# Performance work log

Measured on AMD Instinct MI355X. Metric: run time of the kernel, lower is better.

Reference implementation:

```python
import jax, jax.numpy as jnp
import numpy as np

N, IN_CH, OUT_CH = 8192, 128, 64

def setup_inputs() -> dict:
    key = jax.random.key(0)
    k1, k2, k3, k4, k5 = jax.random.split(key, 5)
    features = jax.random.normal(k1, (N, IN_CH), dtype=jnp.float32)
    weight_matrix = jax.random.normal(k2, (IN_CH, OUT_CH), dtype=jnp.float32) * (1.0 / np.sqrt(IN_CH))
    filt = jax.random.uniform(k3, (N,), dtype=jnp.float32, minval=0.9, maxval=1.1)
    wavelets = jax.random.normal(k4, (N, N), dtype=jnp.float32) * (1.0 / np.sqrt(N))
    wavelets_inv = jax.random.normal(k5, (N, N), dtype=jnp.float32) * (1.0 / np.sqrt(N))
    return {"features": features, "weight_matrix": weight_matrix, "filt": filt,
            "wavelets": wavelets, "wavelets_inv": wavelets_inv}

def reference(features, weight_matrix, filt, wavelets, wavelets_inv):
    # transformed = features @ W                      [N, out_ch]
    transformed = features @ weight_matrix
    # spectral = wavelets_inv @ transformed           [N, out_ch]
    spectral = wavelets_inv @ transformed
    # wavelets @ diag(filt) == wavelets * filt[None, :] (fused broadcast,
    # mathematically identical to the original dense-diag GEMM)
    out = (wavelets * filt[None, :]) @ spectral
    return out
```

## Files before the change

### kernel.cpp

```cpp
#include <hip/hip_runtime.h>
#include <hip/hip_bf16.h>


typedef unsigned short u16;
typedef short s16x8 __attribute__((ext_vector_type(8)));
typedef float f32x4 __attribute__((ext_vector_type(4)));

__device__ __forceinline__ u16 f2bf(float f) {
    unsigned u;
    __builtin_memcpy(&u, &f, 4);
    unsigned r = (u + 0x7fffu + ((u >> 16) & 1u)) >> 16;
    return (u16)r;
}
__device__ __forceinline__ unsigned pk2(float a, float b) {
    __hip_bfloat162 h = __float22bfloat162_rn(float2{a, b});
    unsigned u;
    __builtin_memcpy(&u, &h, 4);
    return u;
}

#define GAS(p) ((const __attribute__((address_space(1))) void*)(p))
#define LAS(p) ((__attribute__((address_space(3))) void*)(p))

#define NN 8192
#define MT 64
#define BK 64

__global__ __launch_bounds__(256) void k1_feat(const float* __restrict__ F,
                                               const float* __restrict__ W,
                                               float* __restrict__ Tmp) {
    const int tid = threadIdx.x;
    const int col = tid & 63;
    const int rq = tid >> 6;
    const int row0 = blockIdx.x * 16 + rq * 4;
    float a0 = 0.f, a1 = 0.f, a2 = 0.f, a3 = 0.f;
    const float* f0 = F + (size_t)row0 * 128;
    for (int k = 0; k < 128; ++k) {
        float wv = W[k * 64 + col];
        a0 += f0[k] * wv;
        a1 += f0[128 + k] * wv;
        a2 += f0[256 + k] * wv;
        a3 += f0[384 + k] * wv;
    }
    Tmp[(size_t)(row0 + 0) * 64 + col] = a0;
    Tmp[(size_t)(row0 + 1) * 64 + col] = a1;
    Tmp[(size_t)(row0 + 2) * 64 + col] = a2;
    Tmp[(size_t)(row0 + 3) * 64 + col] = a3;
}

__global__ __launch_bounds__(256) void k2_transpose(const float* __restrict__ Tmp,
                                                    u16* __restrict__ Tt) {
    __shared__ u16 s[64][65];
    const int tid = threadIdx.x;
    const int r0 = blockIdx.x * 64;
    const int c = tid & 63, r = tid >> 6;
#pragma unroll
    for (int p = 0; p < 16; ++p)
        s[r + p * 4][c] = f2bf(Tmp[(size_t)(r0 + r + p * 4) * 64 + c]);
    __syncthreads();
    const int j = tid & 63, nq = tid >> 6;
#pragma unroll
    for (int p = 0; p < 16; ++p) {
        int n = nq + p * 4;
        Tt[(size_t)n * NN + r0 + j] = s[j][n];
    }
}

__global__ __launch_bounds__(256) void gemm_af32_bt(const float* __restrict__ A,
                                                    const u16* __restrict__ Bt,
                                                    float* __restrict__ P,
                                                    int kslice) {
    __shared__ __align__(16) u16 As[MT * BK];
    __shared__ __align__(16) u16 Bs[MT * BK];
    const int tid = threadIdx.x;
    const int w = tid >> 6;
    const int l = tid & 63;
    const int m0 = blockIdx.x * MT;
    const int s = blockIdx.y;
    const int k0 = s * kslice;

    f32x4 acc[4] = {f32x4{0,0,0,0}, f32x4{0,0,0,0}, f32x4{0,0,0,0}, f32x4{0,0,0,0}};

    const int ar = tid >> 2;
    const int ac = tid & 3;
    const float* Ap = A + (size_t)(m0 + ar) * NN + (size_t)k0 + ac * 16;
    u16* Arow = As + ar * 64;
    const int g0 = (2 * ac) ^ (ar & 7);
    const int g1 = (2 * ac + 1) ^ (ar & 7);

    const int lr = l >> 3;
    const int lc = (l & 7) ^ lr;
    const u16* Bb = Bt + (size_t)(w * 16 + lr) * NN + lc * 8 + k0;
    char* BsB = (char*)Bs + (w * 16) * 128;

    const int fm = w * 16 + (l & 15);
    const int q = l >> 4;

    for (int kt = 0; kt < kslice; kt += BK) {
        __builtin_amdgcn_global_load_lds(GAS(Bb + kt), LAS(BsB), 16, 0, 0);
        __builtin_amdgcn_global_load_lds(GAS(Bb + kt + 8 * NN), LAS(BsB + 1024), 16, 0, 0);
        f32x4 f0 = *(const f32x4*)(Ap + kt);
        f32x4 f1 = *(const f32x4*)(Ap + kt + 4);
        f32x4 f2 = *(const f32x4*)(Ap + kt + 8);
        f32x4 f3 = *(const f32x4*)(Ap + kt + 12);
        uint4 p0{pk2(f0.x, f0.y), pk2(f0.z, f0.w), pk2(f1.x, f1.y), pk2(f1.z, f1.w)};
        uint4 p1{pk2(f2.x, f2.y), pk2(f2.z, f2.w), pk2(f3.x, f3.y), pk2(f3.z, f3.w)};
        *(uint4*)(Arow + g0 * 8) = p0;
        *(uint4*)(Arow + g1 * 8) = p1;
        __syncthreads();
#pragma unroll
        for (int kk = 0; kk < 2; ++kk) {
            const int acg = (kk * 4 + q) ^ (fm & 7);
            s16x8 af = *(const s16x8*)&As[fm * 64 + acg * 8];
#pragma unroll
            for (int ng = 0; ng < 4; ++ng) {
                const int bn = ng * 16 + (l & 15);
                const int bc = (kk * 4 + q) ^ (bn & 7);
                s16x8 bf = *(const s16x8*)&Bs[bn * 64 + bc * 8];
                acc[ng] = __builtin_amdgcn_mfma_f32_16x16x32_bf16(af, bf, acc[ng], 0, 0, 0);
            }
        }
        __syncthreads();
    }

    float* Pp = P + (size_t)s * NN * 64;
    const int row = m0 + w * 16 + (l >> 4) * 4;
    const int col = l & 15;
#pragma unroll
    for (int ng = 0; ng < 4; ++ng)
#pragma unroll
        for (int r = 0; r < 4; ++r)
            Pp[(size_t)(row + r) * 64 + ng * 16 + col] = acc[ng][r];
}

__global__ __launch_bounds__(256) void k4_reduce_scale_t(const float* __restrict__ P,
                                                         const float* __restrict__ filt,
                                                         u16* __restrict__ St,
                                                         int split) {
    __shared__ u16 s[64][65];
    const int tid = threadIdx.x;
    const int j0 = blockIdx.x * 64;
    const int n = tid & 63, jq = tid >> 6;
#pragma unroll 4
    for (int p = 0; p < 16; ++p) {
        int j = jq + p * 4;
        float acc = 0.f;
        for (int t = 0; t < split; ++t)
            acc += P[((size_t)t * NN + j0 + j) * 64 + n];
        acc *= filt[j0 + j];
        s[j][n] = f2bf(acc);
    }
    __syncthreads();
    const int jj = tid & 63, nq = tid >> 6;
#pragma unroll
    for (int p = 0; p < 16; ++p) {
        int nn = nq + p * 4;
        St[(size_t)nn * NN + j0 + jj] = s[jj][nn];
    }
}

__global__ __launch_bounds__(256) void k6_reduce_out(const float* __restrict__ P,
                                                     float* __restrict__ out,
                                                     int split) {
    const int idx = blockIdx.x * 256 + threadIdx.x;
    float acc = 0.f;
    for (int t = 0; t < split; ++t)
        acc += P[(size_t)t * NN * 64 + idx];
    out[idx] = acc;
}

extern "C" void kernel_launch(void* const* d_in, const int* in_sizes, int n_in,
                              void* d_out, int out_size, void* d_ws, size_t ws_size,
                              hipStream_t stream) {
    const float* F    = (const float*)d_in[0];
    const float* W    = (const float*)d_in[1];
    const float* filt = (const float*)d_in[2];
    const float* Wav  = (const float*)d_in[3];
    const float* Winv = (const float*)d_in[4];
    float* out = (float*)d_out;

    char* ws = (char*)d_ws;
    u16* Tt = (u16*)ws;
    u16* St = (u16*)(ws + (1u << 20));
    float* Tmp = (float*)(ws + (2u << 20));
    float* P   = (float*)(ws + (2u << 20));

    size_t per = (size_t)NN * 64 * 4;
    size_t avail = (ws_size > (2u << 20)) ? ws_size - (2u << 20) : per;
    int maxs = (int)(avail / per);
    if (maxs < 1) maxs = 1;
    int split = 1;
    while (split * 2 <= maxs && split < 8) split *= 2;
    int kslice = NN / split;

    k1_feat<<<512, 256, 0, stream>>>(F, W, Tmp);
    k2_transpose<<<128, 256, 0, stream>>>(Tmp, Tt);
    gemm_af32_bt<<<dim3(128, split), 256, 0, stream>>>(Winv, Tt, P, kslice);
    k4_reduce_scale_t<<<128, 256, 0, stream>>>(P, filt, St, split);
    gemm_af32_bt<<<dim3(128, split), 256, 0, stream>>>(Wav, St, P, kslice);
    k6_reduce_out<<<2048, 256, 0, stream>>>(P, out, split);
}
```

Measured before the change: 653.5 us.

## Double-buffer LDS tiles in split-K GEMM and vectorize feature loads

The GEMM main loop now uses two LDS buffers per operand. The next tile's global loads (direct-to-LDS for B, register loads for A) are issued before computing MFMAs on the current tile, so memory latency overlaps compute and one barrier per iteration is removed. The small features@W kernel also reads feature rows with 16-byte vector loads instead of scalar ones. This doubles LDS usage (32KB per block), which may lower occupancy, and keeps A-tile values live in registers across the MFMA section.

```diff
diff --git a/kernel.cpp b/kernel.cpp
--- a/kernel.cpp
+++ b/kernel.cpp
@@ -35,12 +35,19 @@
     const int row0 = blockIdx.x * 16 + rq * 4;
     float a0 = 0.f, a1 = 0.f, a2 = 0.f, a3 = 0.f;
     const float* f0 = F + (size_t)row0 * 128;
-    for (int k = 0; k < 128; ++k) {
-        float wv = W[k * 64 + col];
-        a0 += f0[k] * wv;
-        a1 += f0[128 + k] * wv;
-        a2 += f0[256 + k] * wv;
-        a3 += f0[384 + k] * wv;
+    for (int k = 0; k < 128; k += 4) {
+        f32x4 v0 = *(const f32x4*)(f0 + k);
+        f32x4 v1 = *(const f32x4*)(f0 + 128 + k);
+        f32x4 v2 = *(const f32x4*)(f0 + 256 + k);
+        f32x4 v3 = *(const f32x4*)(f0 + 384 + k);
+#pragma unroll
+        for (int kk = 0; kk < 4; ++kk) {
+            float wv = W[(k + kk) * 64 + col];
+            a0 += v0[kk] * wv;
+            a1 += v1[kk] * wv;
+            a2 += v2[kk] * wv;
+            a3 += v3[kk] * wv;
+        }
     }
     Tmp[(size_t)(row0 + 0) * 64 + col] = a0;
     Tmp[(size_t)(row0 + 1) * 64 + col] = a1;
@@ -70,8 +77,8 @@
                                                     const u16* __restrict__ Bt,
                                                     float* __restrict__ P,
                                                     int kslice) {
-    __shared__ __align__(16) u16 As[MT * BK];
-    __shared__ __align__(16) u16 Bs[MT * BK];
+    __shared__ __align__(16) u16 As[2][MT * BK];
+    __shared__ __align__(16) u16 Bs[2][MT * BK];
     const int tid = threadIdx.x;
     const int w = tid >> 6;
     const int l = tid & 63;
@@ -84,43 +91,71 @@
     const int ar = tid >> 2;
     const int ac = tid & 3;
     const float* Ap = A + (size_t)(m0 + ar) * NN + (size_t)k0 + ac * 16;
-    u16* Arow = As + ar * 64;
+    const int arow = ar * 64;
     const int g0 = (2 * ac) ^ (ar & 7);
     const int g1 = (2 * ac + 1) ^ (ar & 7);
 
     const int lr = l >> 3;
     const int lc = (l & 7) ^ lr;
     const u16* Bb = Bt + (size_t)(w * 16 + lr) * NN + lc * 8 + k0;
-    char* BsB = (char*)Bs + (w * 16) * 128;
+    const int bwoff = (w * 16) * 128;
 
     const int fm = w * 16 + (l & 15);
     const int q = l >> 4;
 
-    for (int kt = 0; kt < kslice; kt += BK) {
-        __builtin_amdgcn_global_load_lds(GAS(Bb + kt), LAS(BsB), 16, 0, 0);
-        __builtin_amdgcn_global_load_lds(GAS(Bb + kt + 8 * NN), LAS(BsB + 1024), 16, 0, 0);
-        f32x4 f0 = *(const f32x4*)(Ap + kt);
-        f32x4 f1 = *(const f32x4*)(Ap + kt + 4);
-        f32x4 f2 = *(const f32x4*)(Ap + kt + 8);
-        f32x4 f3 = *(const f32x4*)(Ap + kt + 12);
+    const int nt = kslice / BK;
+
+    __builtin_amdgcn_global_load_lds(GAS(Bb), LAS((char*)Bs + bwoff), 16, 0, 0);
+    __builtin_amdgcn_global_load_lds(GAS(Bb + 8 * NN), LAS((char*)Bs + bwoff + 1024), 16, 0, 0);
+    {
+        f32x4 f0 = *(const f32x4*)(Ap);
+        f32x4 f1 = *(const f32x4*)(Ap + 4);
+        f32x4 f2 = *(const f32x4*)(Ap + 8);
+        f32x4 f3 = *(const f32x4*)(Ap + 12);
         uint4 p0{pk2(f0.x, f0.y), pk2(f0.z, f0.w), pk2(f1.x, f1.y), pk2(f1.z, f1.w)};
         uint4 p1{pk2(f2.x, f2.y), pk2(f2.z, f2.w), pk2(f3.x, f3.y), pk2(f3.z, f3.w)};
-        *(uint4*)(Arow + g0 * 8) = p0;
-        *(uint4*)(Arow + g1 * 8) = p1;
-        __syncthreads();
+        *(uint4*)(&As[0][arow + g0 * 8]) = p0;
+        *(uint4*)(&As[0][arow + g1 * 8]) = p1;
+    }
+    __syncthreads();
+
+    int cur = 0;
+    for (int t = 0; t < nt; ++t) {
+        const int nxt = cur ^ 1;
+        const bool pre = (t + 1 < nt);
+        f32x4 f0, f1, f2, f3;
+        if (pre) {
+            const int kt = (t + 1) * BK;
+            char* BsB = (char*)Bs + nxt * (MT * BK * 2) + bwoff;
+            __builtin_amdgcn_global_load_lds(GAS(Bb + kt), LAS(BsB), 16, 0, 0);
+            __builtin_amdgcn_global_load_lds(GAS(Bb + kt + 8 * NN), LAS(BsB + 1024), 16, 0, 0);
+            f0 = *(const f32x4*)(Ap + kt);
+            f1 = *(const f32x4*)(Ap + kt + 4);
+            f2 = *(const f32x4*)(Ap + kt + 8);
+            f3 = *(const f32x4*)(Ap + kt + 12);
+        }
+        const u16* Asc = &As[cur][0];
+        const u16* Bsc = &Bs[cur][0];
 #pragma unroll
         for (int kk = 0; kk < 2; ++kk) {
             const int acg = (kk * 4 + q) ^ (fm & 7);
-            s16x8 af = *(const s16x8*)&As[fm * 64 + acg * 8];
+            s16x8 af = *(const s16x8*)&Asc[fm * 64 + acg * 8];
 #pragma unroll
             for (int ng = 0; ng < 4; ++ng) {
                 const int bn = ng * 16 + (l & 15);
                 const int bc = (kk * 4 + q) ^ (bn & 7);
-                s16x8 bf = *(const s16x8*)&Bs[bn * 64 + bc * 8];
+                s16x8 bf = *(const s16x8*)&Bsc[bn * 64 + bc * 8];
                 acc[ng] = __builtin_amdgcn_mfma_f32_16x16x32_bf16(af, bf, acc[ng], 0, 0, 0);
             }
         }
+        if (pre) {
+            uint4 p0{pk2(f0.x, f0.y), pk2(f0.z, f0.w), pk2(f1.x, f1.y), pk2(f1.z, f1.w)};
+            uint4 p1{pk2(f2.x, f2.y), pk2(f2.z, f2.w), pk2(f3.x, f3.y), pk2(f3.z, f3.w)};
+            *(uint4*)(&As[nxt][arow + g0 * 8]) = p0;
+            *(uint4*)(&As[nxt][arow + g1 * 8]) = p1;
+        }
         __syncthreads();
+        cur = nxt;
     }
 
     float* Pp = P + (size_t)s * NN * 64;
```

Result: no change. 646.6 us (-1.1%).

## Load GEMM operands straight to registers with double-buffered prefetch; fuse feature kernels

Applied to the files above, without the earlier changes.

The split-K GEMM drops its shared-memory staging and barriers. Each wave now loads its A rows (fp32, converted to bf16 in registers) and the B columns directly from global memory into MFMA fragments, with a two-stage software prefetch. The feature projection and the transpose/bf16 conversion are merged into one kernel, which removes the intermediate fp32 buffer and one launch. The trade-off is that B fragments are no longer shared through LDS across the block's waves, so each wave issues its own B loads, with strided 16-byte accesses across rows.

```diff
diff --git a/kernel.cpp b/kernel.cpp
--- a/kernel.cpp
+++ b/kernel.cpp
@@ -18,45 +18,41 @@
     __builtin_memcpy(&u, &h, 4);
     return u;
 }
-
-#define GAS(p) ((const __attribute__((address_space(1))) void*)(p))
-#define LAS(p) ((__attribute__((address_space(3))) void*)(p))
+__device__ __forceinline__ s16x8 mk_af(f32x4 x, f32x4 y) {
+    union { unsigned u[4]; s16x8 v; } r;
+    r.u[0] = pk2(x.x, x.y);
+    r.u[1] = pk2(x.z, x.w);
+    r.u[2] = pk2(y.x, y.y);
+    r.u[3] = pk2(y.z, y.w);
+    return r.v;
+}
 
 #define NN 8192
-#define MT 64
-#define BK 64
-
-__global__ __launch_bounds__(256) void k1_feat(const float* __restrict__ F,
-                                               const float* __restrict__ W,
-                                               float* __restrict__ Tmp) {
-    const int tid = threadIdx.x;
-    const int col = tid & 63;
-    const int rq = tid >> 6;
-    const int row0 = blockIdx.x * 16 + rq * 4;
-    float a0 = 0.f, a1 = 0.f, a2 = 0.f, a3 = 0.f;
-    const float* f0 = F + (size_t)row0 * 128;
-    for (int k = 0; k < 128; ++k) {
-        float wv = W[k * 64 + col];
-        a0 += f0[k] * wv;
-        a1 += f0[128 + k] * wv;
-        a2 += f0[256 + k] * wv;
-        a3 += f0[384 + k] * wv;
-    }
-    Tmp[(size_t)(row0 + 0) * 64 + col] = a0;
-    Tmp[(size_t)(row0 + 1) * 64 + col] = a1;
-    Tmp[(size_t)(row0 + 2) * 64 + col] = a2;
-    Tmp[(size_t)(row0 + 3) * 64 + col] = a3;
-}
-
-__global__ __launch_bounds__(256) void k2_transpose(const float* __restrict__ Tmp,
-                                                    u16* __restrict__ Tt) {
+
+__global__ __launch_bounds__(256) void k12_feat_t(const float* __restrict__ F,
+                                                  const float* __restrict__ W,
+                                                  u16* __restrict__ Tt) {
     __shared__ u16 s[64][65];
     const int tid = threadIdx.x;
+    const int c = tid & 63;
+    const int w = tid >> 6;
     const int r0 = blockIdx.x * 64;
-    const int c = tid & 63, r = tid >> 6;
-#pragma unroll
-    for (int p = 0; p < 16; ++p)
-        s[r + p * 4][c] = f2bf(Tmp[(size_t)(r0 + r + p * 4) * 64 + c]);
+    float acc[16];
+#pragma unroll
+    for (int p = 0; p < 16; ++p) acc[p] = 0.f;
+    for (int k = 0; k < 128; k += 4) {
+        float wv[4];
+#pragma unroll
+        for (int kk = 0; kk < 4; ++kk) wv[kk] = W[(k + kk) * 64 + c];
+#pragma unroll
+        for (int p = 0; p < 16; ++p) {
+            f32x4 fv = *(const f32x4*)(F + (size_t)(r0 + w + 4 * p) * 128 + k);
+#pragma unroll
+            for (int kk = 0; kk < 4; ++kk) acc[p] += fv[kk] * wv[kk];
+        }
+    }
+#pragma unroll
+    for (int p = 0; p < 16; ++p) s[w + 4 * p][c] = f2bf(acc[p]);
     __syncthreads();
     const int j = tid & 63, nq = tid >> 6;
 #pragma unroll
@@ -66,71 +62,84 @@
     }
 }
 
-__global__ __launch_bounds__(256) void gemm_af32_bt(const float* __restrict__ A,
-                                                    const u16* __restrict__ Bt,
-                                                    float* __restrict__ P,
-                                                    int kslice) {
-    __shared__ __align__(16) u16 As[MT * BK];
-    __shared__ __align__(16) u16 Bs[MT * BK];
+__global__ __launch_bounds__(256) void gemm_direct(const float* __restrict__ A,
+                                                   const u16* __restrict__ Bt,
+                                                   float* __restrict__ P,
+                                                   int kslice) {
     const int tid = threadIdx.x;
     const int w = tid >> 6;
     const int l = tid & 63;
-    const int m0 = blockIdx.x * MT;
+    const int m0 = blockIdx.x * 64;
     const int s = blockIdx.y;
     const int k0 = s * kslice;
 
-    f32x4 acc[4] = {f32x4{0,0,0,0}, f32x4{0,0,0,0}, f32x4{0,0,0,0}, f32x4{0,0,0,0}};
-
-    const int ar = tid >> 2;
-    const int ac = tid & 3;
-    const float* Ap = A + (size_t)(m0 + ar) * NN + (size_t)k0 + ac * 16;
-    u16* Arow = As + ar * 64;
-    const int g0 = (2 * ac) ^ (ar & 7);
-    const int g1 = (2 * ac + 1) ^ (ar & 7);
-
-    const int lr = l >> 3;
-    const int lc = (l & 7) ^ lr;
-    const u16* Bb = Bt + (size_t)(w * 16 + lr) * NN + lc * 8 + k0;
-    char* BsB = (char*)Bs + (w * 16) * 128;
-
-    const int fm = w * 16 + (l & 15);
-    const int q = l >> 4;
-
-    for (int kt = 0; kt < kslice; kt += BK) {
-        __builtin_amdgcn_global_load_lds(GAS(Bb + kt), LAS(BsB), 16, 0, 0);
-        __builtin_amdgcn_global_load_lds(GAS(Bb + kt + 8 * NN), LAS(BsB + 1024), 16, 0, 0);
-        f32x4 f0 = *(const f32x4*)(Ap + kt);
-        f32x4 f1 = *(const f32x4*)(Ap + kt + 4);
-        f32x4 f2 = *(const f32x4*)(Ap + kt + 8);
-        f32x4 f3 = *(const f32x4*)(Ap + kt + 12);
-        uint4 p0{pk2(f0.x, f0.y), pk2(f0.z, f0.w), pk2(f1.x, f1.y), pk2(f1.z, f1.w)};
-        uint4 p1{pk2(f2.x, f2.y), pk2(f2.z, f2.w), pk2(f3.x, f3.y), pk2(f3.z, f3.w)};
-        *(uint4*)(Arow + g0 * 8) = p0;
-        *(uint4*)(Arow + g1 * 8) = p1;
-        __syncthreads();
-#pragma unroll
-        for (int kk = 0; kk < 2; ++kk) {
-            const int acg = (kk * 4 + q) ^ (fm & 7);
-            s16x8 af = *(const s16x8*)&As[fm * 64 + acg * 8];
-#pragma unroll
-            for (int ng = 0; ng < 4; ++ng) {
-                const int bn = ng * 16 + (l & 15);
-                const int bc = (kk * 4 + q) ^ (bn & 7);
-                s16x8 bf = *(const s16x8*)&Bs[bn * 64 + bc * 8];
-                acc[ng] = __builtin_amdgcn_mfma_f32_16x16x32_bf16(af, bf, acc[ng], 0, 0, 0);
-            }
-        }
-        __syncthreads();
-    }
-
+    const int row = m0 + w * 16 + (l & 15);
+    const int kq = (l >> 4) * 8;
+
+    const float* Ap = A + (size_t)row * NN + k0 + kq;
+    const u16* B0 = Bt + (size_t)(l & 15) * NN + k0 + kq;
+    const u16* B1 = B0 + (size_t)16 * NN;
+    const u16* B2 = B0 + (size_t)32 * NN;
+    const u16* B3 = B0 + (size_t)48 * NN;
+
+    f32x4 acc0{0, 0, 0, 0}, acc1{0, 0, 0, 0}, acc2{0, 0, 0, 0}, acc3{0, 0, 0, 0};
+
+    const int nt = kslice / 32;
+
+    f32x4 aA0, aA1, aB0, aB1;
+    s16x8 bA0, bA1, bA2, bA3, bB0, bB1, bB2, bB3;
+
+    aA0 = *(const f32x4*)(Ap + 0);
+    aA1 = *(const f32x4*)(Ap + 4);
+    bA0 = *(const s16x8*)(B0 + 0);
+    bA1 = *(const s16x8*)(B1 + 0);
+    bA2 = *(const s16x8*)(B2 + 0);
+    bA3 = *(const s16x8*)(B3 + 0);
+
+    for (int t = 0; t < nt; t += 2) {
+        {
+            const int o = (t + 1) * 32;
+            aB0 = *(const f32x4*)(Ap + o);
+            aB1 = *(const f32x4*)(Ap + o + 4);
+            bB0 = *(const s16x8*)(B0 + o);
+            bB1 = *(const s16x8*)(B1 + o);
+            bB2 = *(const s16x8*)(B2 + o);
+            bB3 = *(const s16x8*)(B3 + o);
+        }
+        {
+            s16x8 af = mk_af(aA0, aA1);
+            acc0 = __builtin_amdgcn_mfma_f32_16x16x32_bf16(af, bA0, acc0, 0, 0, 0);
+            acc1 = __builtin_amdgcn_mfma_f32_16x16x32_bf16(af, bA1, acc1, 0, 0, 0);
+            acc2 = __builtin_amdgcn_mfma_f32_16x16x32_bf16(af, bA2, acc2, 0, 0, 0);
+            acc3 = __builtin_amdgcn_mfma_f32_16x16x32_bf16(af, bA3, acc3, 0, 0, 0);
+        }
+        if (t + 2 < nt) {
+            const int o = (t + 2) * 32;
+            aA0 = *(const f32x4*)(Ap + o);
+            aA1 = *(const f32x4*)(Ap + o + 4);
+            bA0 = *(const s16x8*)(B0 + o);
+            bA1 = *(const s16x8*)(B1 + o);
+            bA2 = *(const s16x8*)(B2 + o);
+            bA3 = *(const s16x8*)(B3 + o);
+        }
+        {
+            s16x8 af = mk_af(aB0, aB1);
+            acc0 = __builtin_amdgcn_mfma_f32_16x16x32_bf16(af, bB0, acc0, 0, 0, 0);
+            acc1 = __builtin_amdgcn_mfma_f32_16x16x32_bf16(af, bB1, acc1, 0, 0, 0);
+            acc2 = __builtin_amdgcn_mfma_f32_16x16x32_bf16(af, bB2, acc2, 0, 0, 0);
+            acc3 = __builtin_amdgcn_mfma_f32_16x16x32_bf16(af, bB3, acc3, 0, 0, 0);
+        }
+    }
+
+    f32x4 accs[4] = {acc0, acc1, acc2, acc3};
     float* Pp = P + (size_t)s * NN * 64;
-    const int row = m0 + w * 16 + (l >> 4) * 4;
-    const int col = l & 15;
+    const int orow = m0 + w * 16 + (l >> 4) * 4;
+    const int ocol = l & 15;
 #pragma unroll
     for (int ng = 0; ng < 4; ++ng)
 #pragma unroll
         for (int r = 0; r < 4; ++r)
-            Pp[(size_t)(row + r) * 64 + ng * 16 + col] = acc[ng][r];
+            Pp[(size_t)(orow + r) * 64 + ng * 16 + ocol] = accs[ng][r];
 }
 
 __global__ __launch_bounds__(256) void k4_reduce_scale_t(const float* __restrict__ P,
@@ -182,8 +191,7 @@
     char* ws = (char*)d_ws;
     u16* Tt = (u16*)ws;
     u16* St = (u16*)(ws + (1u << 20));
-    float* Tmp = (float*)(ws + (2u << 20));
-    float* P   = (float*)(ws + (2u << 20));
+    float* P = (float*)(ws + (2u << 20));
 
     size_t per = (size_t)NN * 64 * 4;
     size_t avail = (ws_size > (2u << 20)) ? ws_size - (2u << 20) : per;
@@ -193,10 +201,9 @@
     while (split * 2 <= maxs && split < 8) split *= 2;
     int kslice = NN / split;
 
-    k1_feat<<<512, 256, 0, stream>>>(F, W, Tmp);
-    k2_transpose<<<128, 256, 0, stream>>>(Tmp, Tt);
-    gemm_af32_bt<<<dim3(128, split), 256, 0, stream>>>(Winv, Tt, P, kslice);
+    k12_feat_t<<<128, 256, 0, stream>>>(F, W, Tt);
+    gemm_direct<<<dim3(128, split), 256, 0, stream>>>(Winv, Tt, P, kslice);
     k4_reduce_scale_t<<<128, 256, 0, stream>>>(P, filt, St, split);
-    gemm_af32_bt<<<dim3(128, split), 256, 0, stream>>>(Wav, St, P, kslice);
+    gemm_direct<<<dim3(128, split), 256, 0, stream>>>(Wav, St, P, kslice);
     k6_reduce_out<<<2048, 256, 0, stream>>>(P, out, split);
 }
```

New measurement: 701.4 us. 7.3% more time.
